# Kernel tuning notes

Measured on AMD Instinct MI355X. Metric: run time of the kernel, lower is better.

## Reference

```python
import jax, jax.numpy as jnp
import numpy as np

B, S, D, H = 2, 2048, 768, 12
DK = D // H


def setup_inputs() -> dict:
    key = jax.random.key(0)
    ks = jax.random.split(key, 12)
    inp = {
        "q": jax.random.normal(ks[0], (B, S, D), jnp.float32),
        "k": jax.random.normal(ks[1], (B, S, D), jnp.float32),
        "v": jax.random.normal(ks[2], (B, S, D), jnp.float32),
        # float mask: 1.0 where attention is disallowed (causal upper triangle)
        "mask": (1.0 - jnp.tril(jnp.ones((S, S), jnp.float32)))[None, None],
        "Wq": jax.random.normal(ks[3], (D, D), jnp.float32) / np.sqrt(D),
        "bq": jnp.zeros((D,), jnp.float32),
        "Wk": jax.random.normal(ks[4], (D, D), jnp.float32) / np.sqrt(D),
        "bk": jnp.zeros((D,), jnp.float32),
        "Wv": jax.random.normal(ks[5], (D, D), jnp.float32) / np.sqrt(D),
        "bv": jnp.zeros((D,), jnp.float32),
        "Wo": jax.random.normal(ks[6], (D, D), jnp.float32) / np.sqrt(D),
        "bo": jnp.zeros((D,), jnp.float32),
    }
    return inp


def _split_heads(x):
    # [B,S,D] -> [B,H,S,DK]
    b, s, _ = x.shape
    return x.reshape(b, s, H, DK).transpose(0, 2, 1, 3)


def reference(q, k, v, mask, Wq, bq, Wk, bk, Wv, bv, Wo, bo):
    Q = _split_heads(q @ Wq + bq)
    K = _split_heads(k @ Wk + bk)
    V = _split_heads(v @ Wv + bv)
    scale = jax.lax.rsqrt(jnp.float32(D))  # note: d_model, not d_k (faithful)
    logits = jnp.einsum("bhqd,bhkd->bhqk", Q, K) * scale
    logits = logits + (-1e9) * mask
    weights = jax.nn.softmax(logits, axis=-1)
    attn = jnp.einsum("bhqk,bhkd->bhqd", weights, V)
    attn = attn.transpose(0, 2, 1, 3).reshape(q.shape)  # [B,S,D]
    return jax.nn.relu(attn @ Wo + bo)
```

## Files before the change

kernel.cpp:

```cpp
#include <hip/hip_runtime.h>
#include <math.h>

#define BB 2
#define SS 2048
#define DD 768
#define HH 12
#define DKK 64
#define MM (BB*SS)

typedef _Float16 half_t;
using half8 = __attribute__((ext_vector_type(8))) _Float16;
using half4 = __attribute__((ext_vector_type(4))) _Float16;
using floatx4 = __attribute__((ext_vector_type(4))) float;

__device__ __forceinline__ void gload_lds16(const half_t* g, half_t* l)
{
    auto gp = (const __attribute__((address_space(1))) half_t*)(uintptr_t)g;
    auto lp = (__attribute__((address_space(3))) half_t*)(uint32_t)(uintptr_t)l;
    __builtin_amdgcn_global_load_lds(gp, lp, 16, 0, 0);
}

__global__ __launch_bounds__(256)
void convert_qkv(const float* __restrict__ q, const float* __restrict__ k,
                 const float* __restrict__ v, half_t* __restrict__ qh,
                 half_t* __restrict__ kh, half_t* __restrict__ vh)
{
    const float* src = blockIdx.y == 0 ? q : (blockIdx.y == 1 ? k : v);
    half_t* dst      = blockIdx.y == 0 ? qh : (blockIdx.y == 1 ? kh : vh);
    int i = blockIdx.x * 256 + threadIdx.x;
    float4 f = ((const float4*)src)[i];
    half4 hv;
    hv[0] = (half_t)f.x; hv[1] = (half_t)f.y; hv[2] = (half_t)f.z; hv[3] = (half_t)f.w;
    ((half4*)dst)[i] = hv;
}

__global__ __launch_bounds__(256)
void wtrans(const float* __restrict__ W0, const float* __restrict__ W1,
            const float* __restrict__ W2, const float* __restrict__ W3,
            half_t* __restrict__ T0, half_t* __restrict__ T1,
            half_t* __restrict__ T2, half_t* __restrict__ T3)
{
    int z = blockIdx.z;
    const float* W = z == 0 ? W0 : z == 1 ? W1 : z == 2 ? W2 : W3;
    half_t* T      = z == 0 ? T0 : z == 1 ? T1 : z == 2 ? T2 : T3;

    __shared__ float tile[64][68];
    int k0 = blockIdx.x * 64, n0 = blockIdx.y * 64;
    int t = threadIdx.x;
    #pragma unroll
    for (int i = 0; i < 4; ++i) {
        int c = t + i * 256;
        int kr = c >> 4, nc = (c & 15) * 4;
        *(float4*)&tile[kr][nc] = *(const float4*)&W[(size_t)(k0 + kr) * DD + n0 + nc];
    }
    __syncthreads();
    #pragma unroll
    for (int i = 0; i < 4; ++i) {
        int c = t + i * 256;
        int nr = c >> 4, kc = (c & 15) * 4;
        half4 hv;
        #pragma unroll
        for (int j = 0; j < 4; ++j) hv[j] = (half_t)tile[kc + j][nr];
        *(half4*)&T[(size_t)(n0 + nr) * DD + k0 + kc] = hv;
    }
}

template<bool SWAP>
__device__ __forceinline__
void gemm_body(const half_t* __restrict__ A, const half_t* __restrict__ Bt,
               floatx4 (&acc)[4][4], half_t (*As)[32], half_t (*Bs)[32],
               int m0, int n0)
{
    const int t = threadIdx.x;
    const int lane = t & 63, wave = t >> 6;
    const int lr = lane & 15, lq = lane >> 4;
    const int wm = (wave >> 1) * 64, wn = (wave & 1) * 64;
    const int srow0 = wave * 32 + (lane >> 2);
    const int scol  = (lane & 3) * 8;

    #pragma unroll
    for (int mi = 0; mi < 4; ++mi)
        #pragma unroll
        for (int ni = 0; ni < 4; ++ni)
            #pragma unroll
            for (int r = 0; r < 4; ++r) acc[mi][ni][r] = 0.f;

    for (int k0 = 0; k0 < DD; k0 += 32) {
        __syncthreads();
        #pragma unroll
        for (int j = 0; j < 2; ++j) {
            int row = srow0 + j * 16;
            gload_lds16(&A [(size_t)(m0 + row) * DD + k0 + scol], &As[row][scol]);
            gload_lds16(&Bt[(size_t)(n0 + row) * DD + k0 + scol], &Bs[row][scol]);
        }
        __builtin_amdgcn_s_waitcnt(0x0f70);
        __syncthreads();

        half8 af[4], bf[4];
        #pragma unroll
        for (int i = 0; i < 4; ++i) {
            af[i] = *(const half8*)&As[wm + i * 16 + lr][lq * 8];
            bf[i] = *(const half8*)&Bs[wn + i * 16 + lr][lq * 8];
        }
        #pragma unroll
        for (int mi = 0; mi < 4; ++mi)
            #pragma unroll
            for (int ni = 0; ni < 4; ++ni) {
                if (SWAP)
                    acc[mi][ni] = __builtin_amdgcn_mfma_f32_16x16x32_f16(
                        bf[ni], af[mi], acc[mi][ni], 0, 0, 0);
                else
                    acc[mi][ni] = __builtin_amdgcn_mfma_f32_16x16x32_f16(
                        af[mi], bf[ni], acc[mi][ni], 0, 0, 0);
            }
    }
}

__global__ __launch_bounds__(256)
void proj_gemm(const half_t* __restrict__ qh, const half_t* __restrict__ kh,
               const half_t* __restrict__ vh,
               const half_t* __restrict__ Wqt, const half_t* __restrict__ Wkt,
               const half_t* __restrict__ Wvt,
               const float* __restrict__ bq, const float* __restrict__ bk,
               const float* __restrict__ bv,
               half_t* __restrict__ Qo, half_t* __restrict__ Ko,
               half_t* __restrict__ Vto)
{
    const int z = blockIdx.z;
    const half_t* A  = z == 0 ? qh  : z == 1 ? kh  : vh;
    const half_t* Bt = z == 0 ? Wqt : z == 1 ? Wkt : Wvt;
    const float* bias = z == 0 ? bq : z == 1 ? bk : bv;

    __shared__ half_t As[128][32];
    __shared__ half_t Bs[128][32];
    floatx4 acc[4][4];
    const int m0 = blockIdx.y * 128, n0 = blockIdx.x * 128;

    if (z == 2) gemm_body<true >(A, Bt, acc, As, Bs, m0, n0);
    else        gemm_body<false>(A, Bt, acc, As, Bs, m0, n0);

    const int lane = threadIdx.x & 63, wave = threadIdx.x >> 6;
    const int lr = lane & 15, lq = lane >> 4;
    const int wm = (wave >> 1) * 64, wn = (wave & 1) * 64;

    if (z == 2) {
        #pragma unroll
        for (int mi = 0; mi < 4; ++mi)
            #pragma unroll
            for (int ni = 0; ni < 4; ++ni)
                #pragma unroll
                for (int r = 0; r < 4; ++r) {
                    int dcol = n0 + wn + ni * 16 + lq * 4 + r;
                    int srow = m0 + wm + mi * 16 + lr;
                    int hh = dcol >> 6, d = dcol & 63;
                    int b2 = srow >> 11, sdx = srow & 2047;
                    Vto[((size_t)((b2 * HH + hh) * DKK + d)) * SS + sdx] =
                        (half_t)(acc[mi][ni][r] + bias[dcol]);
                }
    } else {
        const float sc = (z == 0) ? 0.03608439182435161f : 1.0f;
        half_t* O = z == 0 ? Qo : Ko;
        #pragma unroll
        for (int mi = 0; mi < 4; ++mi)
            #pragma unroll
            for (int ni = 0; ni < 4; ++ni)
                #pragma unroll
                for (int r = 0; r < 4; ++r) {
                    int row = m0 + wm + mi * 16 + lq * 4 + r;
                    int col = n0 + wn + ni * 16 + lr;
                    O[(size_t)row * DD + col] = (half_t)((acc[mi][ni][r] + bias[col]) * sc);
                }
    }
}

__global__ __launch_bounds__(256)
void out_gemm(const half_t* __restrict__ A, const half_t* __restrict__ Bt,
              const float* __restrict__ bias, float* __restrict__ C)
{
    __shared__ half_t As[128][32];
    __shared__ half_t Bs[128][32];
    floatx4 acc[4][4];
    const int m0 = blockIdx.y * 128, n0 = blockIdx.x * 128;
    gemm_body<false>(A, Bt, acc, As, Bs, m0, n0);

    const int lane = threadIdx.x & 63, wave = threadIdx.x >> 6;
    const int lr = lane & 15, lq = lane >> 4;
    const int wm = (wave >> 1) * 64, wn = (wave & 1) * 64;

    #pragma unroll
    for (int mi = 0; mi < 4; ++mi)
        #pragma unroll
        for (int ni = 0; ni < 4; ++ni)
            #pragma unroll
            for (int r = 0; r < 4; ++r) {
                int row = m0 + wm + mi * 16 + lq * 4 + r;
                int col = n0 + wn + ni * 16 + lr;
                C[(size_t)row * DD + col] = fmaxf(acc[mi][ni][r] + bias[col], 0.f);
            }
}

__global__ __launch_bounds__(128)
void attn_split(const half_t* __restrict__ Qf, const half_t* __restrict__ Kf,
                const half_t* __restrict__ Vt, half_t* __restrict__ Of,
                float* __restrict__ Opart, float* __restrict__ Lpart)
{
    __shared__ half_t Ks[64][72];
    __shared__ half_t Vs[64][72];
    __shared__ half_t Ps[2][32][72];

    const int i = blockIdx.x;
    const int bh = i % 24;
    const int j = i / 24;
    int qt, c; bool single;
    if (j < 16) { qt = 15 - j; c = 0; single = true; }
    else        { int jj = j - 16; qt = 31 - (jj >> 1); c = jj & 1; single = false; }
    const int kt0 = c * 16;
    const int kt1 = (!single && c == 0) ? 16 : (qt + 1);

    const int b = bh / HH, h = bh % HH;
    const int t = threadIdx.x;
    const int lane = t & 63, wave = t >> 6;
    const int lr = lane & 15, lq = lane >> 4;
    const int q0 = qt * 64;

    half8 qa[2][2];
    #pragma unroll
    for (int qg = 0; qg < 2; ++qg) {
        const half_t* qptr =
            Qf + ((size_t)(b * SS + q0 + wave * 32 + qg * 16 + lr)) * DD + h * DKK;
        qa[qg][0] = *(const half8*)(qptr + lq * 8);
        qa[qg][1] = *(const half8*)(qptr + 32 + lq * 8);
    }

    floatx4 o[2][4];
    #pragma unroll
    for (int qg = 0; qg < 2; ++qg)
        #pragma unroll
        for (int nt = 0; nt < 4; ++nt)
            #pragma unroll
            for (int r = 0; r < 4; ++r) o[qg][nt][r] = 0.f;
    float l_run[2] = {0.f, 0.f};

    for (int kt = kt0; kt < kt1; ++kt) {
        __syncthreads();
        #pragma unroll
        for (int ii = 0; ii < 4; ++ii) {
            int cc = t + ii * 128;
            int row = cc >> 3, c8 = (cc & 7) * 8;
            *(half8*)&Ks[row][c8] =
                *(const half8*)&Kf[((size_t)(b * SS + kt * 64 + row)) * DD + h * DKK + c8];
            *(half8*)&Vs[row][c8] =
                *(const half8*)&Vt[((size_t)((b * HH + h) * DKK + row)) * SS + kt * 64 + c8];
        }
        __syncthreads();

        floatx4 s[2][4];
        #pragma unroll
        for (int nt = 0; nt < 4; ++nt) {
            half8 kf0 = *(const half8*)&Ks[nt * 16 + lr][lq * 8];
            half8 kf1 = *(const half8*)&Ks[nt * 16 + lr][32 + lq * 8];
            #pragma unroll
            for (int qg = 0; qg < 2; ++qg) {
                floatx4 a = {0.f, 0.f, 0.f, 0.f};
                a = __builtin_amdgcn_mfma_f32_16x16x32_f16(kf0, qa[qg][0], a, 0, 0, 0);
                a = __builtin_amdgcn_mfma_f32_16x16x32_f16(kf1, qa[qg][1], a, 0, 0, 0);
                s[qg][nt] = a;
            }
        }

        if (kt == qt) {
            #pragma unroll
            for (int qg = 0; qg < 2; ++qg) {
                int qrow = q0 + wave * 32 + qg * 16 + lr;
                #pragma unroll
                for (int nt = 0; nt < 4; ++nt)
                    #pragma unroll
                    for (int r = 0; r < 4; ++r) {
                        int key = kt * 64 + nt * 16 + lq * 4 + r;
                        if (key > qrow) s[qg][nt][r] = -1e30f;
                    }
            }
        }

        #pragma unroll
        for (int qg = 0; qg < 2; ++qg)
            #pragma unroll
            for (int nt = 0; nt < 4; ++nt) {
                half4 hp;
                #pragma unroll
                for (int r = 0; r < 4; ++r) {
                    float p = __expf(s[qg][nt][r]);
                    l_run[qg] += p;
                    hp[r] = (half_t)p;
                }
                *(half4*)&Ps[wave][qg * 16 + lr][nt * 16 + lq * 4] = hp;
            }

        __builtin_amdgcn_s_waitcnt(0xc07f);

        half8 pa[2][2];
        #pragma unroll
        for (int qg = 0; qg < 2; ++qg) {
            pa[qg][0] = *(const half8*)&Ps[wave][qg * 16 + lr][lq * 8];
            pa[qg][1] = *(const half8*)&Ps[wave][qg * 16 + lr][32 + lq * 8];
        }

        #pragma unroll
        for (int nt = 0; nt < 4; ++nt) {
            half8 vf0 = *(const half8*)&Vs[nt * 16 + lr][lq * 8];
            half8 vf1 = *(const half8*)&Vs[nt * 16 + lr][32 + lq * 8];
            #pragma unroll
            for (int qg = 0; qg < 2; ++qg) {
                o[qg][nt] = __builtin_amdgcn_mfma_f32_16x16x32_f16(vf0, pa[qg][0], o[qg][nt], 0, 0, 0);
                o[qg][nt] = __builtin_amdgcn_mfma_f32_16x16x32_f16(vf1, pa[qg][1], o[qg][nt], 0, 0, 0);
            }
        }
    }

    #pragma unroll
    for (int qg = 0; qg < 2; ++qg) {
        l_run[qg] += __shfl_xor(l_run[qg], 16);
        l_run[qg] += __shfl_xor(l_run[qg], 32);
    }

    if (single) {
        #pragma unroll
        for (int qg = 0; qg < 2; ++qg) {
            float inv = 1.f / l_run[qg];
            int qrow = q0 + wave * 32 + qg * 16 + lr;
            #pragma unroll
            for (int nt = 0; nt < 4; ++nt) {
                half4 hv;
                #pragma unroll
                for (int r = 0; r < 4; ++r) hv[r] = (half_t)(o[qg][nt][r] * inv);
                *(half4*)&Of[((size_t)(b * SS + qrow)) * DD + h * DKK + nt * 16 + lq * 4] = hv;
            }
        }
    } else {
        const int p = (bh * 16 + (qt - 16)) * 2 + c;
        float* Ob = Opart + (size_t)p * 4096;
        #pragma unroll
        for (int qg = 0; qg < 2; ++qg) {
            int qq = wave * 32 + qg * 16 + lr;
            #pragma unroll
            for (int nt = 0; nt < 4; ++nt)
                *(floatx4*)&Ob[qq * 64 + nt * 16 + lq * 4] = o[qg][nt];
            if (lq == 0) Lpart[p * 64 + qq] = l_run[qg];
        }
    }
}

__global__ __launch_bounds__(256)
void attn_combine(const float* __restrict__ Opart, const float* __restrict__ Lpart,
                  half_t* __restrict__ Of)
{
    const int ib = blockIdx.x;
    const int bh = ib >> 4, qtm = ib & 15;
    const int b = bh / HH, h = bh % HH;
    const int p0 = (bh * 16 + qtm) * 2, p1 = p0 + 1;
    const int t = threadIdx.x;
    const int q = t >> 2, ds0 = (t & 3) * 16;

    float inv = 1.f / (Lpart[p0 * 64 + q] + Lpart[p1 * 64 + q]);
    const float* O0 = Opart + (size_t)p0 * 4096 + q * 64 + ds0;
    const float* O1 = Opart + (size_t)p1 * 4096 + q * 64 + ds0;
    int srow = (qtm + 16) * 64 + q;
    half_t* dst = Of + ((size_t)(b * SS + srow)) * DD + h * DKK + ds0;

    #pragma unroll
    for (int kk = 0; kk < 4; ++kk) {
        float4 a = *(const float4*)&O0[kk * 4];
        float4 c = *(const float4*)&O1[kk * 4];
        half4 hv;
        hv[0] = (half_t)((a.x + c.x) * inv);
        hv[1] = (half_t)((a.y + c.y) * inv);
        hv[2] = (half_t)((a.z + c.z) * inv);
        hv[3] = (half_t)((a.w + c.w) * inv);
        *(half4*)&dst[kk * 4] = hv;
    }
}

extern "C" void kernel_launch(void* const* d_in, const int* in_sizes, int n_in,
                              void* d_out, int out_size, void* d_ws, size_t ws_size,
                              hipStream_t stream)
{
    (void)in_sizes; (void)n_in; (void)out_size; (void)ws_size;
    const float* q  = (const float*)d_in[0];
    const float* k  = (const float*)d_in[1];
    const float* v  = (const float*)d_in[2];
    const float* Wq = (const float*)d_in[4];
    const float* bq = (const float*)d_in[5];
    const float* Wk = (const float*)d_in[6];
    const float* bk = (const float*)d_in[7];
    const float* Wv = (const float*)d_in[8];
    const float* bv = (const float*)d_in[9];
    const float* Wo = (const float*)d_in[10];
    const float* bo = (const float*)d_in[11];
    float* out = (float*)d_out;

    half_t* qh  = (half_t*)d_ws;
    half_t* kh  = qh  + (size_t)MM * DD;
    half_t* vh  = kh  + (size_t)MM * DD;
    half_t* Wqt = vh  + (size_t)MM * DD;
    half_t* Wkt = Wqt + (size_t)DD * DD;
    half_t* Wvt = Wkt + (size_t)DD * DD;
    half_t* Wot = Wvt + (size_t)DD * DD;
    half_t* Qo  = Wot + (size_t)DD * DD;
    half_t* Ko  = Qo  + (size_t)MM * DD;
    half_t* Vto = Ko  + (size_t)MM * DD;
    half_t* Ao  = Vto + (size_t)MM * DD;

    float* Opart = (float*)d_ws;
    float* Lpart = Opart + (size_t)768 * 4096;

    convert_qkv<<<dim3(MM * DD / 4 / 256, 3), 256, 0, stream>>>(q, k, v, qh, kh, vh);
    wtrans<<<dim3(DD / 64, DD / 64, 4), 256, 0, stream>>>(Wq, Wk, Wv, Wo, Wqt, Wkt, Wvt, Wot);
    proj_gemm<<<dim3(DD / 128, MM / 128, 3), 256, 0, stream>>>(
        qh, kh, vh, Wqt, Wkt, Wvt, bq, bk, bv, Qo, Ko, Vto);
    attn_split<<<dim3(24 * 48), 128, 0, stream>>>(Qo, Ko, Vto, Ao, Opart, Lpart);
    attn_combine<<<dim3(384), 256, 0, stream>>>(Opart, Lpart, Ao);
    out_gemm<<<dim3(DD / 128, MM / 128), 256, 0, stream>>>(Ao, Wot, bo, out);
}
```

Baseline: 242.5 us.

## Retile GEMMs to 64x64 blocks and prefetch K/V tiles in attention

The projection and output GEMMs switch from 128x128 tiles with 256 threads and a K-step of 32 to 64x64 tiles with 128 threads, a K-step of 64 and padded LDS rows. The direct global-to-LDS loads are replaced by ordinary vector loads. This launches many more blocks, for better CU coverage on the small GEMMs, at the cost of less reuse per block. The attention kernel moves from 2 waves handling 32 query rows each to 4 waves handling 16 rows each. It also prefetches the next K/V tile into registers while computing the current one, to overlap global loads with MFMA work at the cost of extra registers.

```diff
diff --git a/kernel.cpp b/kernel.cpp
--- a/kernel.cpp
+++ b/kernel.cpp
@@ -12,13 +12,6 @@
 using half8 = __attribute__((ext_vector_type(8))) _Float16;
 using half4 = __attribute__((ext_vector_type(4))) _Float16;
 using floatx4 = __attribute__((ext_vector_type(4))) float;
-
-__device__ __forceinline__ void gload_lds16(const half_t* g, half_t* l)
-{
-    auto gp = (const __attribute__((address_space(1))) half_t*)(uintptr_t)g;
-    auto lp = (__attribute__((address_space(3))) half_t*)(uint32_t)(uintptr_t)l;
-    __builtin_amdgcn_global_load_lds(gp, lp, 16, 0, 0);
-}
 
 __global__ __launch_bounds__(256)
 void convert_qkv(const float* __restrict__ q, const float* __restrict__ k,
@@ -67,56 +60,63 @@
 
 template<bool SWAP>
 __device__ __forceinline__
-void gemm_body(const half_t* __restrict__ A, const half_t* __restrict__ Bt,
-               floatx4 (&acc)[4][4], half_t (*As)[32], half_t (*Bs)[32],
-               int m0, int n0)
+void gemm_body64(const half_t* __restrict__ A, const half_t* __restrict__ Bt,
+                 floatx4 (&acc)[2][4], half_t (*As)[72], half_t (*Bs)[72],
+                 int m0, int n0)
 {
     const int t = threadIdx.x;
     const int lane = t & 63, wave = t >> 6;
     const int lr = lane & 15, lq = lane >> 4;
-    const int wm = (wave >> 1) * 64, wn = (wave & 1) * 64;
-    const int srow0 = wave * 32 + (lane >> 2);
-    const int scol  = (lane & 3) * 8;
-
-    #pragma unroll
-    for (int mi = 0; mi < 4; ++mi)
+    const int wm = wave * 32;
+    const int srow = t >> 3;
+    const int scol = (t & 7) * 8;
+
+    #pragma unroll
+    for (int mi = 0; mi < 2; ++mi)
         #pragma unroll
         for (int ni = 0; ni < 4; ++ni)
             #pragma unroll
             for (int r = 0; r < 4; ++r) acc[mi][ni][r] = 0.f;
 
-    for (int k0 = 0; k0 < DD; k0 += 32) {
+    for (int k0 = 0; k0 < DD; k0 += 64) {
         __syncthreads();
         #pragma unroll
-        for (int j = 0; j < 2; ++j) {
-            int row = srow0 + j * 16;
-            gload_lds16(&A [(size_t)(m0 + row) * DD + k0 + scol], &As[row][scol]);
-            gload_lds16(&Bt[(size_t)(n0 + row) * DD + k0 + scol], &Bs[row][scol]);
-        }
-        __builtin_amdgcn_s_waitcnt(0x0f70);
+        for (int ii = 0; ii < 4; ++ii) {
+            int row = srow + ii * 16;
+            *(half8*)&As[row][scol] = *(const half8*)&A [(size_t)(m0 + row) * DD + k0 + scol];
+            *(half8*)&Bs[row][scol] = *(const half8*)&Bt[(size_t)(n0 + row) * DD + k0 + scol];
+        }
         __syncthreads();
 
-        half8 af[4], bf[4];
-        #pragma unroll
-        for (int i = 0; i < 4; ++i) {
-            af[i] = *(const half8*)&As[wm + i * 16 + lr][lq * 8];
-            bf[i] = *(const half8*)&Bs[wn + i * 16 + lr][lq * 8];
-        }
-        #pragma unroll
-        for (int mi = 0; mi < 4; ++mi)
-            #pragma unroll
-            for (int ni = 0; ni < 4; ++ni) {
-                if (SWAP)
-                    acc[mi][ni] = __builtin_amdgcn_mfma_f32_16x16x32_f16(
-                        bf[ni], af[mi], acc[mi][ni], 0, 0, 0);
-                else
-                    acc[mi][ni] = __builtin_amdgcn_mfma_f32_16x16x32_f16(
-                        af[mi], bf[ni], acc[mi][ni], 0, 0, 0);
-            }
-    }
-}
-
-__global__ __launch_bounds__(256)
+        half8 af[2][2], bf[4][2];
+        #pragma unroll
+        for (int mi = 0; mi < 2; ++mi)
+            #pragma unroll
+            for (int kp = 0; kp < 2; ++kp)
+                af[mi][kp] = *(const half8*)&As[wm + mi * 16 + lr][kp * 32 + lq * 8];
+        #pragma unroll
+        for (int ni = 0; ni < 4; ++ni)
+            #pragma unroll
+            for (int kp = 0; kp < 2; ++kp)
+                bf[ni][kp] = *(const half8*)&Bs[ni * 16 + lr][kp * 32 + lq * 8];
+
+        #pragma unroll
+        for (int mi = 0; mi < 2; ++mi)
+            #pragma unroll
+            for (int ni = 0; ni < 4; ++ni)
+                #pragma unroll
+                for (int kp = 0; kp < 2; ++kp) {
+                    if (SWAP)
+                        acc[mi][ni] = __builtin_amdgcn_mfma_f32_16x16x32_f16(
+                            bf[ni][kp], af[mi][kp], acc[mi][ni], 0, 0, 0);
+                    else
+                        acc[mi][ni] = __builtin_amdgcn_mfma_f32_16x16x32_f16(
+                            af[mi][kp], bf[ni][kp], acc[mi][ni], 0, 0, 0);
+                }
+    }
+}
+
+__global__ __launch_bounds__(128)
 void proj_gemm(const half_t* __restrict__ qh, const half_t* __restrict__ kh,
                const half_t* __restrict__ vh,
                const half_t* __restrict__ Wqt, const half_t* __restrict__ Wkt,
@@ -131,29 +131,29 @@
     const half_t* Bt = z == 0 ? Wqt : z == 1 ? Wkt : Wvt;
     const float* bias = z == 0 ? bq : z == 1 ? bk : bv;
 
-    __shared__ half_t As[128][32];
-    __shared__ half_t Bs[128][32];
-    floatx4 acc[4][4];
-    const int m0 = blockIdx.y * 128, n0 = blockIdx.x * 128;
-
-    if (z == 2) gemm_body<true >(A, Bt, acc, As, Bs, m0, n0);
-    else        gemm_body<false>(A, Bt, acc, As, Bs, m0, n0);
+    __shared__ half_t As[64][72];
+    __shared__ half_t Bs[64][72];
+    floatx4 acc[2][4];
+    const int m0 = blockIdx.y * 64, n0 = blockIdx.x * 64;
+
+    if (z == 2) gemm_body64<true >(A, Bt, acc, As, Bs, m0, n0);
+    else        gemm_body64<false>(A, Bt, acc, As, Bs, m0, n0);
 
     const int lane = threadIdx.x & 63, wave = threadIdx.x >> 6;
     const int lr = lane & 15, lq = lane >> 4;
-    const int wm = (wave >> 1) * 64, wn = (wave & 1) * 64;
+    const int wm = wave * 32;
 
     if (z == 2) {
         #pragma unroll
-        for (int mi = 0; mi < 4; ++mi)
+        for (int mi = 0; mi < 2; ++mi)
             #pragma unroll
             for (int ni = 0; ni < 4; ++ni)
                 #pragma unroll
                 for (int r = 0; r < 4; ++r) {
-                    int dcol = n0 + wn + ni * 16 + lq * 4 + r;
-                    int srow = m0 + wm + mi * 16 + lr;
+                    int dcol = n0 + ni * 16 + lq * 4 + r;
+                    int srow2 = m0 + wm + mi * 16 + lr;
                     int hh = dcol >> 6, d = dcol & 63;
-                    int b2 = srow >> 11, sdx = srow & 2047;
+                    int b2 = srow2 >> 11, sdx = srow2 & 2047;
                     Vto[((size_t)((b2 * HH + hh) * DKK + d)) * SS + sdx] =
                         (half_t)(acc[mi][ni][r] + bias[dcol]);
                 }
@@ -161,52 +161,52 @@
         const float sc = (z == 0) ? 0.03608439182435161f : 1.0f;
         half_t* O = z == 0 ? Qo : Ko;
         #pragma unroll
-        for (int mi = 0; mi < 4; ++mi)
+        for (int mi = 0; mi < 2; ++mi)
             #pragma unroll
             for (int ni = 0; ni < 4; ++ni)
                 #pragma unroll
                 for (int r = 0; r < 4; ++r) {
                     int row = m0 + wm + mi * 16 + lq * 4 + r;
-                    int col = n0 + wn + ni * 16 + lr;
+                    int col = n0 + ni * 16 + lr;
                     O[(size_t)row * DD + col] = (half_t)((acc[mi][ni][r] + bias[col]) * sc);
                 }
     }
 }
 
-__global__ __launch_bounds__(256)
+__global__ __launch_bounds__(128)
 void out_gemm(const half_t* __restrict__ A, const half_t* __restrict__ Bt,
               const float* __restrict__ bias, float* __restrict__ C)
 {
-    __shared__ half_t As[128][32];
-    __shared__ half_t Bs[128][32];
-    floatx4 acc[4][4];
-    const int m0 = blockIdx.y * 128, n0 = blockIdx.x * 128;
-    gemm_body<false>(A, Bt, acc, As, Bs, m0, n0);
+    __shared__ half_t As[64][72];
+    __shared__ half_t Bs[64][72];
+    floatx4 acc[2][4];
+    const int m0 = blockIdx.y * 64, n0 = blockIdx.x * 64;
+    gemm_body64<false>(A, Bt, acc, As, Bs, m0, n0);
 
     const int lane = threadIdx.x & 63, wave = threadIdx.x >> 6;
     const int lr = lane & 15, lq = lane >> 4;
-    const int wm = (wave >> 1) * 64, wn = (wave & 1) * 64;
-
-    #pragma unroll
-    for (int mi = 0; mi < 4; ++mi)
+    const int wm = wave * 32;
+
+    #pragma unroll
+    for (int mi = 0; mi < 2; ++mi)
         #pragma unroll
         for (int ni = 0; ni < 4; ++ni)
             #pragma unroll
             for (int r = 0; r < 4; ++r) {
                 int row = m0 + wm + mi * 16 + lq * 4 + r;
-                int col = n0 + wn + ni * 16 + lr;
+                int col = n0 + ni * 16 + lr;
                 C[(size_t)row * DD + col] = fmaxf(acc[mi][ni][r] + bias[col], 0.f);
             }
 }
 
-__global__ __launch_bounds__(128)
+__global__ __launch_bounds__(256)
 void attn_split(const half_t* __restrict__ Qf, const half_t* __restrict__ Kf,
                 const half_t* __restrict__ Vt, half_t* __restrict__ Of,
                 float* __restrict__ Opart, float* __restrict__ Lpart)
 {
     __shared__ half_t Ks[64][72];
     __shared__ half_t Vs[64][72];
-    __shared__ half_t Ps[2][32][72];
+    __shared__ half_t Ps[4][16][72];
 
     const int i = blockIdx.x;
     const int bh = i % 24;
@@ -223,130 +223,122 @@
     const int lr = lane & 15, lq = lane >> 4;
     const int q0 = qt * 64;
 
-    half8 qa[2][2];
-    #pragma unroll
-    for (int qg = 0; qg < 2; ++qg) {
-        const half_t* qptr =
-            Qf + ((size_t)(b * SS + q0 + wave * 32 + qg * 16 + lr)) * DD + h * DKK;
-        qa[qg][0] = *(const half8*)(qptr + lq * 8);
-        qa[qg][1] = *(const half8*)(qptr + 32 + lq * 8);
-    }
-
-    floatx4 o[2][4];
-    #pragma unroll
-    for (int qg = 0; qg < 2; ++qg)
-        #pragma unroll
-        for (int nt = 0; nt < 4; ++nt)
-            #pragma unroll
-            for (int r = 0; r < 4; ++r) o[qg][nt][r] = 0.f;
-    float l_run[2] = {0.f, 0.f};
+    const int srow = t >> 3;
+    const int scol = (t & 7) * 8;
+
+    const half_t* Kbase = Kf + (size_t)(b * SS) * DD + h * DKK;
+    const half_t* Vbase = Vt + (size_t)((b * HH + h) * DKK) * SS;
+
+    half8 kpre[2], vpre[2];
+    #pragma unroll
+    for (int ii = 0; ii < 2; ++ii) {
+        int row = srow + ii * 32;
+        kpre[ii] = *(const half8*)&Kbase[(size_t)(kt0 * 64 + row) * DD + scol];
+        vpre[ii] = *(const half8*)&Vbase[(size_t)row * SS + kt0 * 64 + scol];
+    }
+
+    half8 qa[2];
+    {
+        const half_t* qptr = Qf + (size_t)(b * SS + q0 + wave * 16 + lr) * DD + h * DKK;
+        qa[0] = *(const half8*)(qptr + lq * 8);
+        qa[1] = *(const half8*)(qptr + 32 + lq * 8);
+    }
+
+    floatx4 o[4];
+    #pragma unroll
+    for (int nt = 0; nt < 4; ++nt)
+        #pragma unroll
+        for (int r = 0; r < 4; ++r) o[nt][r] = 0.f;
+    float l_run = 0.f;
 
     for (int kt = kt0; kt < kt1; ++kt) {
         __syncthreads();
         #pragma unroll
-        for (int ii = 0; ii < 4; ++ii) {
-            int cc = t + ii * 128;
-            int row = cc >> 3, c8 = (cc & 7) * 8;
-            *(half8*)&Ks[row][c8] =
-                *(const half8*)&Kf[((size_t)(b * SS + kt * 64 + row)) * DD + h * DKK + c8];
-            *(half8*)&Vs[row][c8] =
-                *(const half8*)&Vt[((size_t)((b * HH + h) * DKK + row)) * SS + kt * 64 + c8];
+        for (int ii = 0; ii < 2; ++ii) {
+            int row = srow + ii * 32;
+            *(half8*)&Ks[row][scol] = kpre[ii];
+            *(half8*)&Vs[row][scol] = vpre[ii];
         }
         __syncthreads();
 
-        floatx4 s[2][4];
+        if (kt + 1 < kt1) {
+            #pragma unroll
+            for (int ii = 0; ii < 2; ++ii) {
+                int row = srow + ii * 32;
+                kpre[ii] = *(const half8*)&Kbase[(size_t)((kt + 1) * 64 + row) * DD + scol];
+                vpre[ii] = *(const half8*)&Vbase[(size_t)row * SS + (kt + 1) * 64 + scol];
+            }
+        }
+
+        floatx4 s[4];
         #pragma unroll
         for (int nt = 0; nt < 4; ++nt) {
             half8 kf0 = *(const half8*)&Ks[nt * 16 + lr][lq * 8];
             half8 kf1 = *(const half8*)&Ks[nt * 16 + lr][32 + lq * 8];
-            #pragma unroll
-            for (int qg = 0; qg < 2; ++qg) {
-                floatx4 a = {0.f, 0.f, 0.f, 0.f};
-                a = __builtin_amdgcn_mfma_f32_16x16x32_f16(kf0, qa[qg][0], a, 0, 0, 0);
-                a = __builtin_amdgcn_mfma_f32_16x16x32_f16(kf1, qa[qg][1], a, 0, 0, 0);
-                s[qg][nt] = a;
-            }
+            floatx4 a = {0.f, 0.f, 0.f, 0.f};
+            a = __builtin_amdgcn_mfma_f32_16x16x32_f16(kf0, qa[0], a, 0, 0, 0);
+            a = __builtin_amdgcn_mfma_f32_16x16x32_f16(kf1, qa[1], a, 0, 0, 0);
+            s[nt] = a;
         }
 
         if (kt == qt) {
-            #pragma unroll
-            for (int qg = 0; qg < 2; ++qg) {
-                int qrow = q0 + wave * 32 + qg * 16 + lr;
-                #pragma unroll
-                for (int nt = 0; nt < 4; ++nt)
-                    #pragma unroll
-                    for (int r = 0; r < 4; ++r) {
-                        int key = kt * 64 + nt * 16 + lq * 4 + r;
-                        if (key > qrow) s[qg][nt][r] = -1e30f;
-                    }
-            }
-        }
-
-        #pragma unroll
-        for (int qg = 0; qg < 2; ++qg)
-            #pragma unroll
-            for (int nt = 0; nt < 4; ++nt) {
-                half4 hp;
+            int qrow = q0 + wave * 16 + lr;
+            #pragma unroll
+            for (int nt = 0; nt < 4; ++nt)
                 #pragma unroll
                 for (int r = 0; r < 4; ++r) {
-                    float p = __expf(s[qg][nt][r]);
-                    l_run[qg] += p;
-                    hp[r] = (half_t)p;
+                    int key = kt * 64 + nt * 16 + lq * 4 + r;
+                    if (key > qrow) s[nt][r] = -1e30f;
                 }
-                *(half4*)&Ps[wave][qg * 16 + lr][nt * 16 + lq * 4] = hp;
+        }
+
+        #pragma unroll
+        for (int nt = 0; nt < 4; ++nt) {
+            half4 hp;
+            #pragma unroll
+            for (int r = 0; r < 4; ++r) {
+                float p = __expf(s[nt][r]);
+                l_run += p;
+                hp[r] = (half_t)p;
             }
+            *(half4*)&Ps[wave][lr][nt * 16 + lq * 4] = hp;
+        }
 
         __builtin_amdgcn_s_waitcnt(0xc07f);
 
-        half8 pa[2][2];
-        #pragma unroll
-        for (int qg = 0; qg < 2; ++qg) {
-            pa[qg][0] = *(const half8*)&Ps[wave][qg * 16 + lr][lq * 8];
-            pa[qg][1] = *(const half8*)&Ps[wave][qg * 16 + lr][32 + lq * 8];
-        }
+        half8 pa0 = *(const half8*)&Ps[wave][lr][lq * 8];
+        half8 pa1 = *(const half8*)&Ps[wave][lr][32 + lq * 8];
 
         #pragma unroll
         for (int nt = 0; nt < 4; ++nt) {
             half8 vf0 = *(const half8*)&Vs[nt * 16 + lr][lq * 8];
             half8 vf1 = *(const half8*)&Vs[nt * 16 + lr][32 + lq * 8];
-            #pragma unroll
-            for (int qg = 0; qg < 2; ++qg) {
-                o[qg][nt] = __builtin_amdgcn_mfma_f32_16x16x32_f16(vf0, pa[qg][0], o[qg][nt], 0, 0, 0);
-                o[qg][nt] = __builtin_amdgcn_mfma_f32_16x16x32_f16(vf1, pa[qg][1], o[qg][nt], 0, 0, 0);
-            }
-        }
-    }
-
-    #pragma unroll
-    for (int qg = 0; qg < 2; ++qg) {
-        l_run[qg] += __shfl_xor(l_run[qg], 16);
-        l_run[qg] += __shfl_xor(l_run[qg], 32);
-    }
+            o[nt] = __builtin_amdgcn_mfma_f32_16x16x32_f16(vf0, pa0, o[nt], 0, 0, 0);
+            o[nt] = __builtin_amdgcn_mfma_f32_16x16x32_f16(vf1, pa1, o[nt], 0, 0, 0);
+        }
+    }
+
+    l_run += __shfl_xor(l_run, 16);
+    l_run += __shfl_xor(l_run, 32);
 
     if (single) {
-        #pragma unroll
-        for (int qg = 0; qg < 2; ++qg) {
-            float inv = 1.f / l_run[qg];
-            int qrow = q0 + wave * 32 + qg * 16 + lr;
-            #pragma unroll
-            for (int nt = 0; nt < 4; ++nt) {
-                half4 hv;
-                #pragma unroll
-                for (int r = 0; r < 4; ++r) hv[r] = (half_t)(o[qg][nt][r] * inv);
-                *(half4*)&Of[((size_t)(b * SS + qrow)) * DD + h * DKK + nt * 16 + lq * 4] = hv;
-            }
+        float inv = 1.f / l_run;
+        int qrow = q0 + wave * 16 + lr;
+        #pragma unroll
+        for (int nt = 0; nt < 4; ++nt) {
+            half4 hv;
+            #pragma unroll
+            for (int r = 0; r < 4; ++r) hv[r] = (half_t)(o[nt][r] * inv);
+            *(half4*)&Of[(size_t)(b * SS + qrow) * DD + h * DKK + nt * 16 + lq * 4] = hv;
         }
     } else {
         const int p = (bh * 16 + (qt - 16)) * 2 + c;
         float* Ob = Opart + (size_t)p * 4096;
-        #pragma unroll
-        for (int qg = 0; qg < 2; ++qg) {
-            int qq = wave * 32 + qg * 16 + lr;
-            #pragma unroll
-            for (int nt = 0; nt < 4; ++nt)
-                *(floatx4*)&Ob[qq * 64 + nt * 16 + lq * 4] = o[qg][nt];
-            if (lq == 0) Lpart[p * 64 + qq] = l_run[qg];
-        }
+        int qq = wave * 16 + lr;
+        #pragma unroll
+        for (int nt = 0; nt < 4; ++nt)
+            *(floatx4*)&Ob[qq * 64 + nt * 16 + lq * 4] = o[nt];
+        if (lq == 0) Lpart[p * 64 + qq] = l_run;
     }
 }
 
@@ -365,7 +357,7 @@
     const float* O0 = Opart + (size_t)p0 * 4096 + q * 64 + ds0;
     const float* O1 = Opart + (size_t)p1 * 4096 + q * 64 + ds0;
     int srow = (qtm + 16) * 64 + q;
-    half_t* dst = Of + ((size_t)(b * SS + srow)) * DD + h * DKK + ds0;
+    half_t* dst = Of + (size_t)(b * SS + srow) * DD + h * DKK + ds0;
 
     #pragma unroll
     for (int kk = 0; kk < 4; ++kk) {
@@ -415,9 +407,9 @@
 
     convert_qkv<<<dim3(MM * DD / 4 / 256, 3), 256, 0, stream>>>(q, k, v, qh, kh, vh);
     wtrans<<<dim3(DD / 64, DD / 64, 4), 256, 0, stream>>>(Wq, Wk, Wv, Wo, Wqt, Wkt, Wvt, Wot);
-    proj_gemm<<<dim3(DD / 128, MM / 128, 3), 256, 0, stream>>>(
+    proj_gemm<<<dim3(DD / 64, MM / 64, 3), 128, 0, stream>>>(
         qh, kh, vh, Wqt, Wkt, Wvt, bq, bk, bv, Qo, Ko, Vto);
-    attn_split<<<dim3(24 * 48), 128, 0, stream>>>(Qo, Ko, Vto, Ao, Opart, Lpart);
+    attn_split<<<dim3(24 * 48), 256, 0, stream>>>(Qo, Ko, Vto, Ao, Opart, Lpart);
     attn_combine<<<dim3(384), 256, 0, stream>>>(Opart, Lpart, Ao);
-    out_gemm<<<dim3(DD / 128, MM / 128), 256, 0, stream>>>(Ao, Wot, bo, out);
-}
+    out_gemm<<<dim3(DD / 64, MM / 64), 128, 0, stream>>>(Ao, Wot, bo, out);
+}
```

New measurement: 207.4 us. 1.17x faster.
